# Optimization experiments

Measured on AMD Instinct MI355X. Metric: run time of the kernel, lower is better.

Reference implementation:

```python
import jax, jax.numpy as jnp
import numpy as np
from jax import lax

WS = 5      # window_size
NH = 8      # num_heads
C = 192     # channels
CPH = (2 * C // 3) // (2 * NH)  # per-head channel dim = 8


def _l2n(x):
    # F.normalize(dim=-1) with eps clamp
    n = jnp.linalg.norm(x, axis=-1, keepdims=True)
    return x / jnp.maximum(n, 1e-12)


def _conv3(x, w, b):
    y = lax.conv_general_dilated(x, w, (1, 1), 'SAME',
                                 dimension_numbers=('NCHW', 'OIHW', 'NCHW'))
    return y + b[None, :, None, None]


def _cpb_bias(cpb_w1, cpb_b1, cpb_w2):
    # relative coords table, Swin-V2 style log-spaced
    rel = np.arange(-(WS - 1), WS, dtype=np.float32)
    tbl = np.stack(np.meshgrid(rel, rel, indexing='ij'), axis=-1)  # (2W-1,2W-1,2)
    tbl = tbl / (WS - 1) * 8.0
    tbl = np.sign(tbl) * np.log2(np.abs(tbl) + 1.0) / np.log2(8.0)
    tbl = jnp.asarray(tbl.reshape(-1, 2))                          # (81,2)
    # relative position index (static int table)
    coords = np.stack(np.meshgrid(np.arange(WS), np.arange(WS), indexing='ij')).reshape(2, -1)
    rc = (coords[:, :, None] - coords[:, None, :]).transpose(1, 2, 0)  # (25,25,2)
    rc[..., 0] += WS - 1
    rc[..., 1] += WS - 1
    rc[..., 0] *= 2 * WS - 1
    idx = rc.sum(-1).reshape(-1)                                    # (625,)
    # cpb MLP: Linear(2,512)+ReLU, Linear(512,NH,no bias)
    h = jax.nn.relu(tbl @ cpb_w1.T + cpb_b1)
    bias_tbl = h @ cpb_w2.T                                         # (81, NH)
    bias = bias_tbl[idx].reshape(WS * WS, WS * WS, NH).transpose(2, 0, 1)
    return 16.0 * jax.nn.sigmoid(bias)                              # (NH,25,25)


def _wa(x, logit_scale, bias):
    # windowed cosine attention; note: scores are K@K^T (faithful to source)
    b, c2, h, w = x.shape
    hb, wb = h // WS, w // WS
    # 'b (kv head c) (h dh) (w dw) -> kv (b h w) head (dh dw) c'
    xr = x.reshape(b, 2, NH, CPH, hb, WS, wb, WS)
    xr = xr.transpose(1, 0, 4, 6, 2, 5, 7, 3).reshape(2, b * hb * wb, NH, WS * WS, CPH)
    k, v = xr[0], xr[1]
    kn = _l2n(k)
    scale = jnp.exp(jnp.minimum(logit_scale, jnp.log(100.0)))       # (NH,1,1)
    atn = jnp.einsum('wnic,wnjc->wnij', kn, kn) * scale + bias[None]
    atn = jax.nn.softmax(atn, axis=-1)
    y = jnp.einsum('wnij,wnjc->wnic', atn, v)                       # (bhw,NH,25,CPH)
    y = y.reshape(b, hb, wb, NH, WS, WS, CPH)
    y = y.transpose(0, 3, 6, 1, 4, 2, 5).reshape(b, NH * CPH, h, w)
    return y


def _forward(x, w_in, b_in, w_out, b_out, logit_scale, lr_logit_scale,
             cpb_w1, cpb_b1, cpb_w2):
    b, c, h, w = x.shape
    xp = _conv3(x, w_in, b_in)                                      # (b, 2c, h, w)
    ch = 2 * c // 3
    x0, x1, x2 = xp[:, :ch], xp[:, ch:2 * ch], xp[:, 2 * ch:]
    bias = _cpb_bias(cpb_w1, cpb_b1, cpb_w2)
    ys = []
    # branch 0: plain window attention
    ys.append(_wa(x0, logit_scale, bias))
    # branch 1: shifted windows (note asymmetric shifts, faithful to torch code)
    x1s = jnp.roll(x1, shift=(-WS // 2, -WS // 2), axis=(2, 3))
    y1 = _wa(x1s, logit_scale, bias)
    y1 = jnp.roll(y1, shift=(WS // 2, WS // 2), axis=(2, 3))
    ys.append(y1)
    # branch 2: long-range axial cosine attention
    xr = x2.reshape(b, 2, NH, CPH, h, w).transpose(1, 0, 4, 2, 5, 3)
    xr = xr.reshape(2, b * h, NH, w, CPH)                           # kv,(b h),head,w,c
    k, v = xr[0], xr[1]
    scale = jnp.exp(jnp.minimum(lr_logit_scale, jnp.log(100.0)))
    kn = _l2n(k)
    atn = jax.nn.softmax(jnp.einsum('bnic,bnjc->bnij', kn, kn) * scale, axis=-1)
    v = jnp.einsum('bnij,bnjc->bnic', atn, v)
    # '(b h) head w c -> (b w) head h c'
    k = k.reshape(b, h, NH, w, CPH).transpose(0, 3, 2, 1, 4).reshape(b * w, NH, h, CPH)
    v = v.reshape(b, h, NH, w, CPH).transpose(0, 3, 2, 1, 4).reshape(b * w, NH, h, CPH)
    kn = _l2n(k)
    atn = jax.nn.softmax(jnp.einsum('bnic,bnjc->bnij', kn, kn) * scale, axis=-1)
    v = jnp.einsum('bnij,bnjc->bnic', atn, v)
    # '(b w) head h c -> b (head c) h w'
    y2 = v.reshape(b, w, NH, h, CPH).transpose(0, 2, 4, 3, 1).reshape(b, NH * CPH, h, w)
    ys.append(y2)
    y = jnp.concatenate(ys, axis=1)                                 # (b, c, h, w)
    return _conv3(y, w_out, b_out)


def setup_inputs() -> dict:
    key = jax.random.key(0)
    ks = jax.random.split(key, 8)
    B, H, W = 2, 160, 160
    s = 0.02
    return {
        'x': jax.random.normal(ks[0], (B, C, H, W), jnp.float32),
        'w_in': jax.random.normal(ks[1], (2 * C, C, 3, 3), jnp.float32) * s,
        'b_in': jnp.zeros((2 * C,), jnp.float32),
        'w_out': jax.random.normal(ks[2], (C, C, 3, 3), jnp.float32) * s,
        'b_out': jnp.zeros((C,), jnp.float32),
        'logit_scale': jnp.log(10.0 * jnp.ones((NH, 1, 1), jnp.float32)),
        'lr_logit_scale': jnp.log(10.0 * jnp.ones((NH, 1, 1), jnp.float32)),
        'cpb_w1': jax.random.normal(ks[3], (512, 2), jnp.float32) * s,
        'cpb_b1': jnp.zeros((512,), jnp.float32),
        'cpb_w2': jax.random.normal(ks[4], (NH, 512), jnp.float32) * s,
    }


def reference(x, w_in, b_in, w_out, b_out, logit_scale, lr_logit_scale,
              cpb_w1, cpb_b1, cpb_w2):
    return _forward(x, w_in, b_in, w_out, b_out, logit_scale, lr_logit_scale,
                    cpb_w1, cpb_b1, cpb_w2)
```

## Files before the change

kernel.cpp:

```cpp
#include <hip/hip_runtime.h>
#include <math.h>


typedef __attribute__((ext_vector_type(8))) short short8;
typedef __attribute__((ext_vector_type(4))) short short4v;
typedef __attribute__((ext_vector_type(4))) float f32x4;

constexpr int Hc = 160, Wc = 160, Bc = 2;
constexpr int HPR = 162;
constexpr int HPW = 164;

__device__ inline unsigned short f2bf(float f) {
  union { float f; unsigned u; } v; v.f = f;
  unsigned r = v.u + 0x7FFF + ((v.u >> 16) & 1);
  return (unsigned short)(r >> 16);
}
__device__ inline float bf2f(unsigned short h) {
  union { unsigned u; float f; } v; v.u = ((unsigned)h) << 16;
  return v.f;
}

__device__ inline void gl16(const void* g, void* l) {
  __builtin_amdgcn_global_load_lds((const __attribute__((address_space(1))) unsigned int*)g,
                                   (__attribute__((address_space(3))) unsigned int*)l, 16, 0, 0);
}

__device__ inline float dot8(f32x4 a0, f32x4 a1, f32x4 b0, f32x4 b1) {
  float d = a0[0] * b0[0];
  d = fmaf(a0[1], b0[1], d); d = fmaf(a0[2], b0[2], d); d = fmaf(a0[3], b0[3], d);
  d = fmaf(a1[0], b1[0], d); d = fmaf(a1[1], b1[1], d);
  d = fmaf(a1[2], b1[2], d); d = fmaf(a1[3], b1[3], d);
  return d;
}

__global__ __launch_bounds__(256)
void prep_kernel(const float* __restrict__ x, unsigned short* __restrict__ xpad,
                 unsigned short* __restrict__ ypad,
                 const float* __restrict__ w_in, unsigned short* __restrict__ wtr1,
                 const float* __restrict__ w_out, unsigned short* __restrict__ wtr2,
                 const float* __restrict__ cw1, const float* __restrict__ cb1,
                 const float* __restrict__ cw2, float* __restrict__ biasf) {
  __shared__ float tile[192][33];
  const int bid = blockIdx.x;
  const int t = threadIdx.x;
  if (bid < 1600) {
    int blk = bid;
    const int w0 = (blk % 5) * 32; blk /= 5;
    const int h = blk % 160;
    const int b = blk / 160;
    for (int i = t; i < 192 * 32; i += 256) {
      int c = i >> 5, w = i & 31;
      tile[c][w] = x[(((size_t)b * 192 + c) * 160 + h) * 160 + w0 + w];
    }
    __syncthreads();
    for (int i = t; i < 32 * 192; i += 256) {
      int w = i / 192, c = i % 192;
      xpad[(((size_t)b * HPR + h + 1) * HPW + w0 + w + 1) * 192 + c] = f2bf(tile[c][w]);
    }
  } else if (bid < 1963) {
    const int NPOS = 968;
    const int total = 2 * 2 * NPOS * 24;
    int idx = (bid - 1600) * 256 + t;
    if (idx >= total) return;
    const int ch = idx % 24; int q = idx / 24;
    const int pos = q % NPOS; q /= NPOS;
    const int b = q & 1; const int buf = q >> 1;
    int row, col;
    if (pos < 328) { row = (pos < 164) ? 0 : 161; col = pos % 164; }
    else { int r = pos - 328; row = 1 + (r >> 2); int cm = r & 3; col = cm == 0 ? 0 : 160 + cm; }
    unsigned short* p = (buf ? ypad : xpad) + (((size_t)b * HPR + row) * HPW + col) * 192 + ch * 8;
    short8 z = {};
    *(short8*)p = z;
  } else if (bid < 2395) {
    const bool first = bid < 2251;
    const int CO = first ? 384 : 192;
    const int NT = CO / 16;
    const float* w = first ? w_in : w_out;
    unsigned short* wtr = first ? wtr1 : wtr2;
    int id = (bid - (first ? 1963 : 2251)) * 256 + t;
    if (id >= CO * 192) return;
    const int co = id / 192, ci = id % 192;
    const int cs = ci >> 5, kh = (ci >> 3) & 3, j = ci & 7;
    const int cotile = co >> 4, cor = co & 15;
    const float* wp = w + (size_t)id * 9;
#pragma unroll
    for (int tap = 0; tap < 9; ++tap)
      wtr[((((size_t)tap * 6 + cs) * NT + cotile) * 64 + kh * 16 + cor) * 8 + j] = f2bf(wp[tap]);
  } else {
    if (t >= 64) return;
    const int e = bid - 2395;
    const int d0 = e / 9, d1 = e % 9;
    const int r0 = d0 - 4, r1 = d1 - 4;
    float t0 = log2f(fabsf((float)r0) * 2.0f + 1.0f) * (1.0f / 3.0f); if (r0 < 0) t0 = -t0;
    float t1 = log2f(fabsf((float)r1) * 2.0f + 1.0f) * (1.0f / 3.0f); if (r1 < 0) t1 = -t1;
    const int lane = t;
    float acc[8];
#pragma unroll
    for (int n = 0; n < 8; ++n) acc[n] = 0.f;
    for (int k = lane; k < 512; k += 64) {
      float hk = fmaf(t0, cw1[k * 2 + 0], fmaf(t1, cw1[k * 2 + 1], cb1[k]));
      hk = fmaxf(hk, 0.f);
#pragma unroll
      for (int n = 0; n < 8; ++n) acc[n] = fmaf(hk, cw2[n * 512 + k], acc[n]);
    }
#pragma unroll
    for (int n = 0; n < 8; ++n) {
#pragma unroll
      for (int off = 32; off > 0; off >>= 1) acc[n] += __shfl_xor(acc[n], off, 64);
    }
    if (lane == 0) {
#pragma unroll
      for (int n = 0; n < 8; ++n)
        biasf[e * 8 + n] = 16.0f / (1.0f + expf(-acc[n]));
    }
  }
}

template<int COUT, int OUTMODE>
__global__ __launch_bounds__(256, 2)
void conv_mfma(const unsigned short* __restrict__ xin, const unsigned short* __restrict__ wtrA,
               const float* __restrict__ bias, unsigned short* __restrict__ obf,
               float* __restrict__ of32) {
  constexpr int CIN = 192;
  constexpr int R = 6;
  constexpr int TOTAL = R * 84 * 4;
  constexpr int SLAB = R * 84 * 32;
  constexpr int NT = COUT / 16;
  __shared__ unsigned short slab[2 * SLAB];
  const int t = threadIdx.x, lane = t & 63, wid = t >> 6;
  const int bx = blockIdx.x, cog = blockIdx.y, b = blockIdx.z;
  const int ws = bx & 1, hb = bx >> 1;
  const int w0 = ws * 80, h0 = hb * 4;
  const int hr = wid;
  const int l15 = lane & 15, l4 = lane >> 4;
  const int co0 = cog * 64;

  f32x4 acc[5][4];
#pragma unroll
  for (int ct = 0; ct < 4; ++ct) {
    f32x4 bi;
#pragma unroll
    for (int r = 0; r < 4; ++r) bi[r] = bias[co0 + ct * 16 + l4 * 4 + r];
#pragma unroll
    for (int mt = 0; mt < 5; ++mt) acc[mt][ct] = bi;
  }

  auto stage = [&](int cs, int bufbase) {
#pragma unroll
    for (int ib0 = 0; ib0 < 8; ++ib0) {
      const int ib = ib0 * 4 + wid;
      const int n = ib * 64 + lane;
      if (n < TOTAL) {
        const int c = n & 3, q = n >> 2;
        const int r = q / 84, wv = q - r * 84;
        const int csrc = c ^ ((wv >> 1) & 3);
        const unsigned short* g = xin +
            (((size_t)b * HPR + h0 + r) * HPW + w0 + wv) * CIN + cs * 32 + csrc * 8;
        gl16(g, &slab[bufbase + ib * 512]);
      }
    }
  };

#define LOADA(a, ky, cs)                                                         \
  {                                                                              \
    _Pragma("unroll")                                                            \
    for (int kx = 0; kx < 3; ++kx) {                                             \
      _Pragma("unroll")                                                          \
      for (int ct = 0; ct < 4; ++ct)                                             \
        a[kx * 4 + ct] = *(const short8*)(wtrA +                                 \
            ((size_t)(((ky) * 3 + kx) * 6 + (cs)) * NT + cog * 4 + ct) * 512 +   \
            lane * 8);                                                           \
    }                                                                            \
  }

#define GROUP(a, ky, bufbase)                                                    \
  {                                                                              \
    const unsigned short* srow = &slab[(bufbase) + (hr + (ky)) * 84 * 32];       \
    _Pragma("unroll")                                                            \
    for (int kx = 0; kx < 3; ++kx) {                                             \
      _Pragma("unroll")                                                          \
      for (int mt = 0; mt < 5; ++mt) {                                           \
        const int wv = mt * 16 + l15 + kx;                                       \
        const int cr = l4 ^ ((wv >> 1) & 3);                                     \
        short8 bf = *(const short8*)(srow + wv * 32 + cr * 8);                   \
        _Pragma("unroll")                                                        \
        for (int ct = 0; ct < 4; ++ct)                                           \
          acc[mt][ct] =                                                          \
              __builtin_amdgcn_mfma_f32_16x16x32_bf16(a[kx * 4 + ct], bf,        \
                                                      acc[mt][ct], 0, 0, 0);     \
      }                                                                          \
    }                                                                            \
  }

#define CSBODY(cs, base, nbase, LAST)                                            \
  {                                                                              \
    if (!(LAST)) stage((cs) + 1, nbase);                                         \
    __builtin_amdgcn_s_setprio(1);                                               \
    GROUP(A0f, 0, base);                                                         \
    __builtin_amdgcn_s_setprio(0);                                               \
    if (!(LAST)) LOADA(A0f, 0, (cs) + 1);                                        \
    __builtin_amdgcn_s_setprio(1);                                               \
    GROUP(A1f, 1, base);                                                         \
    __builtin_amdgcn_s_setprio(0);                                               \
    if (!(LAST)) LOADA(A1f, 1, (cs) + 1);                                        \
    __builtin_amdgcn_s_setprio(1);                                               \
    GROUP(A2f, 2, base);                                                         \
    __builtin_amdgcn_s_setprio(0);                                               \
    if (!(LAST)) {                                                               \
      LOADA(A2f, 2, (cs) + 1);                                                   \
      asm volatile("s_waitcnt vmcnt(36)\n\ts_barrier" ::: "memory");             \
    }                                                                            \
  }

  short8 A0f[12], A1f[12], A2f[12];
  stage(0, 0);
  LOADA(A0f, 0, 0);
  LOADA(A1f, 1, 0);
  LOADA(A2f, 2, 0);
  asm volatile("s_waitcnt vmcnt(36)\n\ts_barrier" ::: "memory");

  CSBODY(0, 0, SLAB, 0);
  CSBODY(1, SLAB, 0, 0);
  CSBODY(2, 0, SLAB, 0);
  CSBODY(3, SLAB, 0, 0);
  CSBODY(4, 0, SLAB, 0);
  CSBODY(5, SLAB, 0, 1);
#undef LOADA
#undef GROUP
#undef CSBODY

  const int h = h0 + hr;
  if (OUTMODE == 0) {
#pragma unroll
    for (int mt = 0; mt < 5; ++mt) {
      const int w = w0 + mt * 16 + l15;
      unsigned short* dst0 = obf + (((size_t)b * Hc + h) * Wc + w) * 384 + co0 + l4 * 4;
#pragma unroll
      for (int ct = 0; ct < 4; ++ct) {
        short4v s;
#pragma unroll
        for (int r = 0; r < 4; ++r) s[r] = (short)f2bf(acc[mt][ct][r]);
        *(short4v*)(dst0 + ct * 16) = s;
      }
    }
  } else {
#pragma unroll
    for (int mt = 0; mt < 5; ++mt) {
      const int w = w0 + mt * 16 + l15;
#pragma unroll
      for (int ct = 0; ct < 4; ++ct)
#pragma unroll
        for (int r = 0; r < 4; ++r) {
          const int co = co0 + ct * 16 + l4 * 4 + r;
          of32[(((size_t)b * COUT + co) * Hc + h) * Wc + w] = acc[mt][ct][r];
        }
    }
  }
}

__global__ __launch_bounds__(256)
void attn1_kernel(const unsigned short* __restrict__ xq, const float* __restrict__ biasf,
                  const float* __restrict__ logit_scale, const float* __restrict__ lrs,
                  unsigned short* __restrict__ ypad, unsigned short* __restrict__ vrow) {
  const int bid = blockIdx.x;
  if (bid < 4096) {
    __shared__ f32x4 kn4[8][25][2];
    __shared__ f32x4 vv4[8][25][2];
    const int head = threadIdx.x >> 5;
    const int i = threadIdx.x & 31;
    const int b = bid >> 11;
    const int r = bid & 2047;
    const int variant = r >> 10;
    const int blk = r & 1023;
    const int chan_off = variant ? 128 : 0;
    const int y_ch_off = variant ? 64 : 0;
    const int shift_in = variant ? 3 : 0;
    const int shift_out = variant ? 2 : 0;
    const int wb_i = blk % 32, hb_i = blk / 32;
    const int wi = i / 5, wj = i % 5;
    const int gh = hb_i * 5 + wi, gw = wb_i * 5 + wj;
    const int sh = (gh + shift_in) % Hc, sw = (gw + shift_in) % Wc;

    if (i < 25) {
      const unsigned short* base = xq + (((size_t)b * Hc + sh) * Wc + sw) * 384 + chan_off + head * 8;
      short8 kv = *(const short8*)base;
      short8 vv = *(const short8*)(base + 64);
      float k[8]; float nrm = 0.f;
#pragma unroll
      for (int c = 0; c < 8; ++c) { k[c] = bf2f((unsigned short)kv[c]); nrm = fmaf(k[c], k[c], nrm); }
      const float inv = 1.0f / fmaxf(sqrtf(nrm), 1e-12f);
      f32x4 a0, a1, b0, b1;
#pragma unroll
      for (int c = 0; c < 4; ++c) { a0[c] = k[c] * inv; a1[c] = k[c + 4] * inv; }
#pragma unroll
      for (int c = 0; c < 4; ++c) { b0[c] = bf2f((unsigned short)vv[c]); b1[c] = bf2f((unsigned short)vv[c + 4]); }
      kn4[head][i][0] = a0; kn4[head][i][1] = a1;
      vv4[head][i][0] = b0; vv4[head][i][1] = b1;
    }
    __syncthreads();
    if (i >= 25) return;

    const float scale = expf(fminf(logit_scale[head], 4.6051702f));
    const f32x4 q0 = kn4[head][i][0], q1 = kn4[head][i][1];
    float s[25];
#pragma unroll
    for (int j = 0; j < 25; ++j) {
      const float d = dot8(q0, q1, kn4[head][j][0], kn4[head][j][1]);
      const int d0 = wi - (j / 5) + 4, d1 = wj - (j % 5) + 4;
      s[j] = fmaf(d, scale, biasf[(d0 * 9 + d1) * 8 + head]);
    }
    float m = -1e30f;
#pragma unroll
    for (int j = 0; j < 25; ++j) m = fmaxf(m, s[j]);
    float den = 0.f;
    f32x4 acc0 = {0.f, 0.f, 0.f, 0.f}, acc1 = {0.f, 0.f, 0.f, 0.f};
#pragma unroll
    for (int j = 0; j < 25; ++j) {
      const float p = __expf(s[j] - m);
      den += p;
      acc0 += vv4[head][j][0] * p;
      acc1 += vv4[head][j][1] * p;
    }
    const float rden = 1.0f / den;
    const int oh = (gh + shift_out) % Hc, ow = (gw + shift_out) % Wc;
    short8 o;
#pragma unroll
    for (int c = 0; c < 4; ++c) { o[c] = (short)f2bf(acc0[c] * rden); o[c + 4] = (short)f2bf(acc1[c] * rden); }
    *(short8*)(ypad + (((size_t)b * HPR + oh + 1) * HPW + ow + 1) * 192 + y_ch_off + head * 8) = o;
  } else {
    __shared__ f32x4 kn4[160][2];
    __shared__ f32x4 vv4[160][2];
    int u = bid - 4096;
    const int head = u % 8; u /= 8;
    const int h = u % 160;
    const int b = u / 160;
    const int i = threadIdx.x;

    if (i < 160) {
      const unsigned short* base = xq + (((size_t)b * Hc + h) * Wc + i) * 384 + 256 + head * 8;
      short8 kv = *(const short8*)base;
      short8 vv = *(const short8*)(base + 64);
      float k[8]; float nrm = 0.f;
#pragma unroll
      for (int c = 0; c < 8; ++c) { k[c] = bf2f((unsigned short)kv[c]); nrm = fmaf(k[c], k[c], nrm); }
      const float inv = 1.0f / fmaxf(sqrtf(nrm), 1e-12f);
      f32x4 a0, a1, b0, b1;
#pragma unroll
      for (int c = 0; c < 4; ++c) { a0[c] = k[c] * inv; a1[c] = k[c + 4] * inv; }
#pragma unroll
      for (int c = 0; c < 4; ++c) { b0[c] = bf2f((unsigned short)vv[c]); b1[c] = bf2f((unsigned short)vv[c + 4]); }
      kn4[i][0] = a0; kn4[i][1] = a1;
      vv4[i][0] = b0; vv4[i][1] = b1;
    }
    __syncthreads();
    if (i >= 160) return;

    const float scale = expf(fminf(lrs[head], 4.6051702f));
    const f32x4 q0 = kn4[i][0], q1 = kn4[i][1];
    float den = 0.f;
    f32x4 acc0 = {0.f, 0.f, 0.f, 0.f}, acc1 = {0.f, 0.f, 0.f, 0.f};
    for (int j = 0; j < 160; ++j) {
      const float d = dot8(q0, q1, kn4[j][0], kn4[j][1]);
      const float p = __expf(fmaf(d, scale, -scale));
      den += p;
      acc0 += vv4[j][0] * p;
      acc1 += vv4[j][1] * p;
    }
    const float rden = 1.0f / den;
    short8 o;
#pragma unroll
    for (int c = 0; c < 4; ++c) { o[c] = (short)f2bf(acc0[c] * rden); o[c + 4] = (short)f2bf(acc1[c] * rden); }
    *(short8*)(vrow + ((((size_t)b * 8 + head) * 160 + h) * 160 + i) * 8) = o;
  }
}

__global__ __launch_bounds__(192)
void col_attn_kernel(const unsigned short* __restrict__ xq, const float* __restrict__ lrs,
                     const unsigned short* __restrict__ vrow, unsigned short* __restrict__ ypad) {
  __shared__ f32x4 kn4[160][2];
  __shared__ f32x4 vv4[160][2];
  int blk = blockIdx.x;
  const int head = blk % 8; blk /= 8;
  const int w = blk % 160; blk /= 160;
  const int b = blk;
  const int i = threadIdx.x;

  if (i < 160) {
    const unsigned short* kb = xq + (((size_t)b * Hc + i) * Wc + w) * 384 + 256 + head * 8;
    short8 kv = *(const short8*)kb;
    short8 vv = *(const short8*)(vrow + ((((size_t)b * 8 + head) * 160 + i) * 160 + w) * 8);
    float k[8]; float nrm = 0.f;
#pragma unroll
    for (int c = 0; c < 8; ++c) { k[c] = bf2f((unsigned short)kv[c]); nrm = fmaf(k[c], k[c], nrm); }
    const float inv = 1.0f / fmaxf(sqrtf(nrm), 1e-12f);
    f32x4 a0, a1, b0, b1;
#pragma unroll
    for (int c = 0; c < 4; ++c) { a0[c] = k[c] * inv; a1[c] = k[c + 4] * inv; }
#pragma unroll
    for (int c = 0; c < 4; ++c) { b0[c] = bf2f((unsigned short)vv[c]); b1[c] = bf2f((unsigned short)vv[c + 4]); }
    kn4[i][0] = a0; kn4[i][1] = a1;
    vv4[i][0] = b0; vv4[i][1] = b1;
  }
  __syncthreads();
  if (i >= 160) return;

  const float scale = expf(fminf(lrs[head], 4.6051702f));
  const f32x4 q0 = kn4[i][0], q1 = kn4[i][1];
  float den = 0.f;
  f32x4 acc0 = {0.f, 0.f, 0.f, 0.f}, acc1 = {0.f, 0.f, 0.f, 0.f};
  for (int j = 0; j < 160; ++j) {
    const float d = dot8(q0, q1, kn4[j][0], kn4[j][1]);
    const float p = __expf(fmaf(d, scale, -scale));
    den += p;
    acc0 += vv4[j][0] * p;
    acc1 += vv4[j][1] * p;
  }
  const float rden = 1.0f / den;
  short8 o;
#pragma unroll
  for (int c = 0; c < 4; ++c) { o[c] = (short)f2bf(acc0[c] * rden); o[c + 4] = (short)f2bf(acc1[c] * rden); }
  *(short8*)(ypad + (((size_t)b * HPR + i + 1) * HPW + w + 1) * 192 + 128 + head * 8) = o;
}

extern "C" void kernel_launch(void* const* d_in, const int* in_sizes, int n_in,
                              void* d_out, int out_size, void* d_ws, size_t ws_size,
                              hipStream_t stream) {
  const float* x     = (const float*)d_in[0];
  const float* w_in  = (const float*)d_in[1];
  const float* b_in  = (const float*)d_in[2];
  const float* w_out = (const float*)d_in[3];
  const float* b_out = (const float*)d_in[4];
  const float* ls    = (const float*)d_in[5];
  const float* lrs   = (const float*)d_in[6];
  const float* cw1   = (const float*)d_in[7];
  const float* cb1   = (const float*)d_in[8];
  const float* cw2   = (const float*)d_in[9];
  float* out = (float*)d_out;

  char* p = (char*)d_ws;
  unsigned short* xpad = (unsigned short*)p;  p += (size_t)Bc * HPR * HPW * 192 * 2;
  unsigned short* ypad = (unsigned short*)p;  p += (size_t)Bc * HPR * HPW * 192 * 2;
  unsigned short* xq   = (unsigned short*)p;  p += (size_t)Bc * Hc * Wc * 384 * 2;
  unsigned short* vrow = (unsigned short*)p;  p += (size_t)Bc * 8 * Hc * Wc * 8 * 2;
  unsigned short* wtr1 = (unsigned short*)p;  p += (size_t)9 * 384 * 192 * 2;
  unsigned short* wtr2 = (unsigned short*)p;  p += (size_t)9 * 192 * 192 * 2;
  float* biasf = (float*)p;

  prep_kernel<<<2476, 256, 0, stream>>>(x, xpad, ypad, w_in, wtr1, w_out, wtr2, cw1, cb1, cw2, biasf);
  conv_mfma<384, 0><<<dim3(80, 6, Bc), 256, 0, stream>>>(xpad, wtr1, b_in, xq, nullptr);
  attn1_kernel<<<4096 + Bc * 160 * 8, 256, 0, stream>>>(xq, biasf, ls, lrs, ypad, vrow);
  col_attn_kernel<<<Bc * 160 * 8, 192, 0, stream>>>(xq, lrs, vrow, ypad);
  conv_mfma<192, 1><<<dim3(80, 3, Bc), 256, 0, stream>>>(ypad, wtr2, b_out, nullptr, out);
}
```

Baseline: 261.3 us.

## Write long-range K/V in head-major layout and batch column attention by four columns

```diff
diff --git a/kernel.cpp b/kernel.cpp
--- a/kernel.cpp
+++ b/kernel.cpp
@@ -120,6 +120,7 @@
 __global__ __launch_bounds__(256, 2)
 void conv_mfma(const unsigned short* __restrict__ xin, const unsigned short* __restrict__ wtrA,
                const float* __restrict__ bias, unsigned short* __restrict__ obf,
+               unsigned short* __restrict__ xk2k, unsigned short* __restrict__ xk2v,
                float* __restrict__ of32) {
   constexpr int CIN = 192;
   constexpr int R = 6;
@@ -231,16 +232,33 @@
 
   const int h = h0 + hr;
   if (OUTMODE == 0) {
-#pragma unroll
-    for (int mt = 0; mt < 5; ++mt) {
-      const int w = w0 + mt * 16 + l15;
-      unsigned short* dst0 = obf + (((size_t)b * Hc + h) * Wc + w) * 384 + co0 + l4 * 4;
-#pragma unroll
-      for (int ct = 0; ct < 4; ++ct) {
-        short4v s;
-#pragma unroll
-        for (int r = 0; r < 4; ++r) s[r] = (short)f2bf(acc[mt][ct][r]);
-        *(short4v*)(dst0 + ct * 16) = s;
+    if (co0 < 256) {
+#pragma unroll
+      for (int mt = 0; mt < 5; ++mt) {
+        const int w = w0 + mt * 16 + l15;
+        unsigned short* dst0 = obf + (((size_t)b * Hc + h) * Wc + w) * 256 + co0 + l4 * 4;
+#pragma unroll
+        for (int ct = 0; ct < 4; ++ct) {
+          short4v s;
+#pragma unroll
+          for (int r = 0; r < 4; ++r) s[r] = (short)f2bf(acc[mt][ct][r]);
+          *(short4v*)(dst0 + ct * 16) = s;
+        }
+      }
+    } else {
+      unsigned short* xk2 = (co0 == 256) ? xk2k : xk2v;
+#pragma unroll
+      for (int mt = 0; mt < 5; ++mt) {
+        const int w = w0 + mt * 16 + l15;
+#pragma unroll
+        for (int ct = 0; ct < 4; ++ct) {
+          const int rel = ct * 16 + l4 * 4;
+          const int head = rel >> 3, within = rel & 7;
+          short4v s;
+#pragma unroll
+          for (int r = 0; r < 4; ++r) s[r] = (short)f2bf(acc[mt][ct][r]);
+          *(short4v*)(xk2 + ((((size_t)b * 8 + head) * 160 + h) * 160 + w) * 8 + within) = s;
+        }
       }
     }
   } else {
@@ -261,13 +279,15 @@
 __global__ __launch_bounds__(256)
 void attn1_kernel(const unsigned short* __restrict__ xq, const float* __restrict__ biasf,
                   const float* __restrict__ logit_scale, const float* __restrict__ lrs,
+                  const unsigned short* __restrict__ xk2k, const unsigned short* __restrict__ xk2v,
                   unsigned short* __restrict__ ypad, unsigned short* __restrict__ vrow) {
   const int bid = blockIdx.x;
   if (bid < 4096) {
     __shared__ f32x4 kn4[8][25][2];
     __shared__ f32x4 vv4[8][25][2];
-    const int head = threadIdx.x >> 5;
-    const int i = threadIdx.x & 31;
+    const int t = threadIdx.x;
+    const int head = t & 7;
+    const int i = t >> 3;
     const int b = bid >> 11;
     const int r = bid & 2047;
     const int variant = r >> 10;
@@ -282,7 +302,7 @@
     const int sh = (gh + shift_in) % Hc, sw = (gw + shift_in) % Wc;
 
     if (i < 25) {
-      const unsigned short* base = xq + (((size_t)b * Hc + sh) * Wc + sw) * 384 + chan_off + head * 8;
+      const unsigned short* base = xq + (((size_t)b * Hc + sh) * Wc + sw) * 256 + chan_off + head * 8;
       short8 kv = *(const short8*)base;
       short8 vv = *(const short8*)(base + 64);
       float k[8]; float nrm = 0.f;
@@ -337,9 +357,9 @@
     const int i = threadIdx.x;
 
     if (i < 160) {
-      const unsigned short* base = xq + (((size_t)b * Hc + h) * Wc + i) * 384 + 256 + head * 8;
-      short8 kv = *(const short8*)base;
-      short8 vv = *(const short8*)(base + 64);
+      const size_t base = ((((size_t)b * 8 + head) * 160 + h) * 160 + i) * 8;
+      short8 kv = *(const short8*)(xk2k + base);
+      short8 vv = *(const short8*)(xk2v + base);
       float k[8]; float nrm = 0.f;
 #pragma unroll
       for (int c = 0; c < 8; ++c) { k[c] = bf2f((unsigned short)kv[c]); nrm = fmaf(k[c], k[c], nrm); }
@@ -374,21 +394,23 @@
   }
 }
 
-__global__ __launch_bounds__(192)
-void col_attn_kernel(const unsigned short* __restrict__ xq, const float* __restrict__ lrs,
+__global__ __launch_bounds__(640)
+void col_attn_kernel(const unsigned short* __restrict__ xk2k, const float* __restrict__ lrs,
                      const unsigned short* __restrict__ vrow, unsigned short* __restrict__ ypad) {
-  __shared__ f32x4 kn4[160][2];
-  __shared__ f32x4 vv4[160][2];
+  __shared__ f32x4 knT[4][161][2];
+  __shared__ f32x4 vvT[4][161][2];
   int blk = blockIdx.x;
-  const int head = blk % 8; blk /= 8;
-  const int w = blk % 160; blk /= 160;
-  const int b = blk;
-  const int i = threadIdx.x;
-
-  if (i < 160) {
-    const unsigned short* kb = xq + (((size_t)b * Hc + i) * Wc + w) * 384 + 256 + head * 8;
-    short8 kv = *(const short8*)kb;
-    short8 vv = *(const short8*)(vrow + ((((size_t)b * 8 + head) * 160 + i) * 160 + w) * 8);
+  const int wg = blk % 40; blk /= 40;
+  const int head = blk % 8;
+  const int b = blk / 8;
+  const int w0 = wg * 4;
+  const int t = threadIdx.x;
+
+  {
+    const int h = t >> 2, wc = t & 3;
+    const size_t base = ((((size_t)b * 8 + head) * 160 + h) * 160 + (w0 + wc)) * 8;
+    short8 kv = *(const short8*)(xk2k + base);
+    short8 vv = *(const short8*)(vrow + base);
     float k[8]; float nrm = 0.f;
 #pragma unroll
     for (int c = 0; c < 8; ++c) { k[c] = bf2f((unsigned short)kv[c]); nrm = fmaf(k[c], k[c], nrm); }
@@ -398,28 +420,28 @@
     for (int c = 0; c < 4; ++c) { a0[c] = k[c] * inv; a1[c] = k[c + 4] * inv; }
 #pragma unroll
     for (int c = 0; c < 4; ++c) { b0[c] = bf2f((unsigned short)vv[c]); b1[c] = bf2f((unsigned short)vv[c + 4]); }
-    kn4[i][0] = a0; kn4[i][1] = a1;
-    vv4[i][0] = b0; vv4[i][1] = b1;
+    knT[wc][h][0] = a0; knT[wc][h][1] = a1;
+    vvT[wc][h][0] = b0; vvT[wc][h][1] = b1;
   }
   __syncthreads();
-  if (i >= 160) return;
-
+
+  const int wi = t / 160, i = t % 160;
   const float scale = expf(fminf(lrs[head], 4.6051702f));
-  const f32x4 q0 = kn4[i][0], q1 = kn4[i][1];
+  const f32x4 q0 = knT[wi][i][0], q1 = knT[wi][i][1];
   float den = 0.f;
   f32x4 acc0 = {0.f, 0.f, 0.f, 0.f}, acc1 = {0.f, 0.f, 0.f, 0.f};
   for (int j = 0; j < 160; ++j) {
-    const float d = dot8(q0, q1, kn4[j][0], kn4[j][1]);
+    const float d = dot8(q0, q1, knT[wi][j][0], knT[wi][j][1]);
     const float p = __expf(fmaf(d, scale, -scale));
     den += p;
-    acc0 += vv4[j][0] * p;
-    acc1 += vv4[j][1] * p;
+    acc0 += vvT[wi][j][0] * p;
+    acc1 += vvT[wi][j][1] * p;
   }
   const float rden = 1.0f / den;
   short8 o;
 #pragma unroll
   for (int c = 0; c < 4; ++c) { o[c] = (short)f2bf(acc0[c] * rden); o[c + 4] = (short)f2bf(acc1[c] * rden); }
-  *(short8*)(ypad + (((size_t)b * HPR + i + 1) * HPW + w + 1) * 192 + 128 + head * 8) = o;
+  *(short8*)(ypad + (((size_t)b * HPR + i + 1) * HPW + w0 + wi + 1) * 192 + 128 + head * 8) = o;
 }
 
 extern "C" void kernel_launch(void* const* d_in, const int* in_sizes, int n_in,
@@ -440,15 +462,17 @@
   char* p = (char*)d_ws;
   unsigned short* xpad = (unsigned short*)p;  p += (size_t)Bc * HPR * HPW * 192 * 2;
   unsigned short* ypad = (unsigned short*)p;  p += (size_t)Bc * HPR * HPW * 192 * 2;
-  unsigned short* xq   = (unsigned short*)p;  p += (size_t)Bc * Hc * Wc * 384 * 2;
+  unsigned short* xq   = (unsigned short*)p;  p += (size_t)Bc * Hc * Wc * 256 * 2;
+  unsigned short* xk2k = (unsigned short*)p;  p += (size_t)Bc * 8 * Hc * Wc * 8 * 2;
+  unsigned short* xk2v = (unsigned short*)p;  p += (size_t)Bc * 8 * Hc * Wc * 8 * 2;
   unsigned short* vrow = (unsigned short*)p;  p += (size_t)Bc * 8 * Hc * Wc * 8 * 2;
   unsigned short* wtr1 = (unsigned short*)p;  p += (size_t)9 * 384 * 192 * 2;
   unsigned short* wtr2 = (unsigned short*)p;  p += (size_t)9 * 192 * 192 * 2;
   float* biasf = (float*)p;
 
   prep_kernel<<<2476, 256, 0, stream>>>(x, xpad, ypad, w_in, wtr1, w_out, wtr2, cw1, cb1, cw2, biasf);
-  conv_mfma<384, 0><<<dim3(80, 6, Bc), 256, 0, stream>>>(xpad, wtr1, b_in, xq, nullptr);
-  attn1_kernel<<<4096 + Bc * 160 * 8, 256, 0, stream>>>(xq, biasf, ls, lrs, ypad, vrow);
-  col_attn_kernel<<<Bc * 160 * 8, 192, 0, stream>>>(xq, lrs, vrow, ypad);
-  conv_mfma<192, 1><<<dim3(80, 3, Bc), 256, 0, stream>>>(ypad, wtr2, b_out, nullptr, out);
-}
+  conv_mfma<384, 0><<<dim3(80, 6, Bc), 256, 0, stream>>>(xpad, wtr1, b_in, xq, xk2k, xk2v, nullptr);
+  attn1_kernel<<<4096 + Bc * 160 * 8, 256, 0, stream>>>(xq, biasf, ls, lrs, xk2k, xk2v, ypad, vrow);
+  col_attn_kernel<<<Bc * 8 * 40, 640, 0, stream>>>(xk2k, lrs, vrow, ypad);
+  conv_mfma<192, 1><<<dim3(80, 3, Bc), 256, 0, stream>>>(ypad, wtr2, b_out, nullptr, nullptr, nullptr, out);
+}
```

After: 239.8 us. 8.2% less time.
